# Kernel optimization log

Measured on AMD Instinct MI355X. Metric: run time of the kernel, lower is better.

## Reference

```python
import jax, jax.numpy as jnp
import numpy as np

N = 100000   # nodes
E = 1600000  # edges (avg degree 16)
D = 128      # hidden_dim


def setup_inputs() -> dict:
    key = jax.random.key(0)
    k1, k2, k3, k4, k5, k6 = jax.random.split(key, 6)
    return {
        "t": jnp.zeros((), dtype=jnp.float32),  # unused by the ODE func
        "x": jax.random.normal(k1, (N, D), dtype=jnp.float32),
        "x0": jax.random.normal(k2, (N, D), dtype=jnp.float32),
        "alpha_train": jax.random.normal(k3, (N,), dtype=jnp.float32),
        "adj_values": jax.random.uniform(k4, (E,), dtype=jnp.float32),
        "adj_row": jax.random.randint(k5, (E,), 0, N, dtype=jnp.int32),
        "adj_col": jax.random.randint(k6, (E,), 0, N, dtype=jnp.int32),
    }


def reference(t, x, x0, alpha_train, adj_values, adj_row, adj_col):
    # alph = sigmoid(alpha_train).unsqueeze(1)  -> [N, 1]
    alph = jax.nn.sigmoid(alpha_train)[:, None]
    # ax = spmm(adj, x): COO gather of source-node features, scale by edge
    # value, scatter-add into destination rows. [N, D]
    ax = jax.ops.segment_sum(adj_values[:, None] * x[adj_col], adj_row,
                             num_segments=x.shape[0])
    # f = alph * 0.5 * (ax - x) + x0
    return alph * 0.5 * (ax - x) + x0
```

## Files before the change

### kernel.cpp

```cpp
#include <hip/hip_runtime.h>


#define DIM 128
#define RPB 64
#define RSHIFT 6
#define ACHUNK 4096
#define BCAP 2048
#define NBMAX 2048
#define HISTB 128

typedef float f2v __attribute__((ext_vector_type(2)));

__device__ __forceinline__ float sigmoidf_(float a) {
    return 1.0f / (1.0f + __expf(-a));
}
__device__ __forceinline__ unsigned f2bf(float f) {
    unsigned u = __float_as_uint(f);
    return (u + 0x7FFFu + ((u >> 16) & 1u)) >> 16;
}

__global__ __launch_bounds__(256)
void xcast_hist_kernel(const float* __restrict__ x,
                       unsigned short* __restrict__ xb, int n4,
                       const int* __restrict__ row, int* __restrict__ bhist,
                       int n_edges, int nb, int xg) {
    __shared__ int h[NBMAX];
    if ((int)blockIdx.x < xg) {
        int i = blockIdx.x * 256 + threadIdx.x;
        if (i >= n4) return;
        float4 v = reinterpret_cast<const float4*>(x)[i];
        uint2 o;
        o.x = f2bf(v.x) | (f2bf(v.y) << 16);
        o.y = f2bf(v.z) | (f2bf(v.w) << 16);
        reinterpret_cast<uint2*>(xb)[i] = o;
        return;
    }
    int t = threadIdx.x;
    int bid = blockIdx.x - xg;
    for (int i = t; i < NBMAX; i += 256) h[i] = 0;
    __syncthreads();
    int e4 = n_edges >> 2;
    for (int i = bid * 256 + t; i < e4; i += HISTB * 256) {
        int4 r = reinterpret_cast<const int4*>(row)[i];
        atomicAdd(&h[r.x >> RSHIFT], 1);
        atomicAdd(&h[r.y >> RSHIFT], 1);
        atomicAdd(&h[r.z >> RSHIFT], 1);
        atomicAdd(&h[r.w >> RSHIFT], 1);
    }
    if (bid == 0 && t == 0) {
        for (int i = e4 << 2; i < n_edges; ++i)
            atomicAdd(&bhist[row[i] >> RSHIFT], 1);
    }
    __syncthreads();
    for (int i = t; i < NBMAX; i += 256)
        if (h[i]) atomicAdd(&bhist[i], h[i]);
}

__global__ __launch_bounds__(1024)
void bucket_scan_kernel(const int* __restrict__ bhist, int* __restrict__ boffs,
                        int* __restrict__ bcur, int nb) {
    __shared__ int ts[1024];
    int t = threadIdx.x;
    int i0 = 2 * t, i1 = 2 * t + 1;
    int v0 = (i0 < nb) ? bhist[i0] : 0;
    int v1 = (i1 < nb) ? bhist[i1] : 0;
    ts[t] = v0 + v1;
    __syncthreads();
    for (int off = 1; off < 1024; off <<= 1) {
        int u = (t >= off) ? ts[t - off] : 0;
        __syncthreads();
        ts[t] += u;
        __syncthreads();
    }
    int ex = (t == 0) ? 0 : ts[t - 1];
    if (i0 < nb) { boffs[i0] = ex;      bcur[i0] = ex; }
    if (i1 < nb) { boffs[i1] = ex + v0; bcur[i1] = ex + v0; }
    if (t == 1023) boffs[nb] = ts[1023];
}

__global__ __launch_bounds__(256)
void bin_kernel(const int* __restrict__ row, const int* __restrict__ col,
                const float* __restrict__ vals, int* __restrict__ bcursor,
                int2* __restrict__ epackA, int n_edges, int nb) {
    __shared__ int hist[NBMAX];
    __shared__ int lbase[NBMAX];
    __shared__ int gbase[NBMAX];
    __shared__ int lcur[NBMAX];
    __shared__ int ts[256];
    __shared__ int2 stage[ACHUNK];
    __shared__ unsigned short bkid[ACHUNK];
    int t = threadIdx.x;
    int base = blockIdx.x * ACHUNK;
    int m = n_edges - base;
    if (m > ACHUNK) m = ACHUNK;
    for (int i = t; i < NBMAX; i += 256) hist[i] = 0;
    __syncthreads();
    for (int i = t; i < m; i += 256)
        atomicAdd(&hist[row[base + i] >> RSHIFT], 1);
    __syncthreads();
    int tb = t * 8;
    int hh[8];
    int run = 0;
#pragma unroll
    for (int j = 0; j < 8; ++j) { hh[j] = hist[tb + j]; run += hh[j]; }
    ts[t] = run;
    __syncthreads();
    for (int off = 1; off < 256; off <<= 1) {
        int u = (t >= off) ? ts[t - off] : 0;
        __syncthreads();
        ts[t] += u;
        __syncthreads();
    }
    int ex = (t == 0) ? 0 : ts[t - 1];
#pragma unroll
    for (int j = 0; j < 8; ++j) { lbase[tb + j] = ex; ex += hh[j]; }
    __syncthreads();
    for (int i = t; i < nb; i += 256) {
        int hv = hist[i];
        gbase[i] = hv ? atomicAdd(&bcursor[i], hv) : 0;
        lcur[i] = 0;
    }
    __syncthreads();
    for (int i = t; i < m; i += 256) {
        int r = row[base + i];
        int c = col[base + i];
        float v = vals[base + i];
        int bk = r >> RSHIFT;
        int lp = atomicAdd(&lcur[bk], 1);
        int sp = lbase[bk] + lp;
        stage[sp] = make_int2(((r & (RPB - 1)) << 17) | c, __float_as_int(v));
        bkid[sp] = (unsigned short)bk;
    }
    __syncthreads();
    for (int i = t; i < m; i += 256) {
        int bk = bkid[i];
        epackA[gbase[bk] + (i - lbase[bk])] = stage[i];
    }
}

template <int USE_BF16>
__global__ __launch_bounds__(512)
void fused_sort_gather_kernel(const unsigned short* __restrict__ xb,
                              const float* __restrict__ x,
                              const float* __restrict__ x0,
                              const float* __restrict__ alpha,
                              const int* __restrict__ boffs,
                              const int2* __restrict__ epackA,
                              float* __restrict__ out, int n_nodes) {
    __shared__ int2 eout[BCAP];
    __shared__ int rowstart[RPB];
    __shared__ int rowcur[RPB];
    __shared__ float sval[RPB];
    int b = blockIdx.x, t = threadIdx.x;
    int r0 = b * RPB;
    int begin = boffs[b], end = boffs[b + 1];
    int n = end - begin;
    if (t < RPB) {
        int r = r0 + t;
        sval[t] = (r < n_nodes) ? 0.5f * sigmoidf_(alpha[r]) : 0.f;
        rowstart[t] = 0;
    }
    __syncthreads();
    int wave = t >> 6, lane = t & 63;
    const unsigned* xbp = reinterpret_cast<const unsigned*>(xb);
    const float2* xp = reinterpret_cast<const float2*>(x);
    const f2v* x0v = reinterpret_cast<const f2v*>(x0);
    f2v* outv = reinterpret_cast<f2v*>(out);
    if (n <= BCAP) {
        for (int i = t; i < n; i += 512)
            atomicAdd(&rowstart[epackA[begin + i].x >> 17], 1);
        __syncthreads();
        if (t < RPB) rowcur[t] = rowstart[t];
        __syncthreads();
        for (int off = 1; off < RPB; off <<= 1) {
            int u = (t < RPB && t >= off) ? rowcur[t - off] : 0;
            __syncthreads();
            if (t < RPB) rowcur[t] += u;
            __syncthreads();
        }
        if (t < RPB) {
            int excl = rowcur[t] - rowstart[t];
            rowstart[t] = excl;
            rowcur[t] = excl;
        }
        __syncthreads();
        for (int i = t; i < n; i += 512) {
            int2 e = epackA[begin + i];
            int pos = atomicAdd(&rowcur[e.x >> 17], 1);
            eout[pos] = make_int2(e.x & 0x1FFFF, e.y);
        }
        __syncthreads();
        for (int q = 0; q < 8; ++q) {
            int lr = wave * 8 + q;
            int r = r0 + lr;
            if (r >= n_nodes) break;
            float s = sval[lr];
            int rb = r * 64;
            f2v a0 = __builtin_nontemporal_load(&x0v[rb + lane]);
            float2 acc = make_float2(a0.x, a0.y);
            if (USE_BF16) {
                unsigned dx = xbp[rb + lane];
                acc.x -= s * __uint_as_float((dx & 0xFFFFu) << 16);
                acc.y -= s * __uint_as_float(dx & 0xFFFF0000u);
            } else {
                float2 xv = xp[rb + lane];
                acc.x -= s * xv.x;
                acc.y -= s * xv.y;
            }
            int k = rowstart[lr];
            int stop = (lr + 1 < RPB) ? rowstart[lr + 1] : n;
            for (; k + 8 <= stop; k += 8) {
                float w[8];
                if (USE_BF16) {
                    unsigned d[8];
#pragma unroll
                    for (int j = 0; j < 8; ++j) {
                        int2 e = eout[k + j];
                        w[j] = s * __int_as_float(e.y);
                        d[j] = xbp[(size_t)e.x * 64 + lane];
                    }
#pragma unroll
                    for (int j = 0; j < 8; ++j) {
                        acc.x += w[j] * __uint_as_float((d[j] & 0xFFFFu) << 16);
                        acc.y += w[j] * __uint_as_float(d[j] & 0xFFFF0000u);
                    }
                } else {
                    float2 v[8];
#pragma unroll
                    for (int j = 0; j < 8; ++j) {
                        int2 e = eout[k + j];
                        w[j] = s * __int_as_float(e.y);
                        v[j] = xp[(size_t)e.x * 64 + lane];
                    }
#pragma unroll
                    for (int j = 0; j < 8; ++j) {
                        acc.x += w[j] * v[j].x;
                        acc.y += w[j] * v[j].y;
                    }
                }
            }
            for (; k < stop; ++k) {
                int2 e = eout[k];
                float w = s * __int_as_float(e.y);
                if (USE_BF16) {
                    unsigned d = xbp[(size_t)e.x * 64 + lane];
                    acc.x += w * __uint_as_float((d & 0xFFFFu) << 16);
                    acc.y += w * __uint_as_float(d & 0xFFFF0000u);
                } else {
                    float2 v = xp[(size_t)e.x * 64 + lane];
                    acc.x += w * v.x;
                    acc.y += w * v.y;
                }
            }
            f2v o; o.x = acc.x; o.y = acc.y;
            __builtin_nontemporal_store(o, &outv[rb + lane]);
        }
    } else {
        for (int q = 0; q < 8; ++q) {
            int lr = wave * 8 + q;
            int r = r0 + lr;
            if (r >= n_nodes) break;
            float s = sval[lr];
            int rb = r * 64;
            float2 acc = reinterpret_cast<const float2*>(x0)[rb + lane];
            if (USE_BF16) {
                unsigned dx = xbp[rb + lane];
                acc.x -= s * __uint_as_float((dx & 0xFFFFu) << 16);
                acc.y -= s * __uint_as_float(dx & 0xFFFF0000u);
            } else {
                float2 xv = xp[rb + lane];
                acc.x -= s * xv.x;
                acc.y -= s * xv.y;
            }
            for (int i = 0; i < n; ++i) {
                int2 e = epackA[begin + i];
                if ((e.x >> 17) == lr) {
                    float w = s * __int_as_float(e.y);
                    if (USE_BF16) {
                        unsigned d = xbp[(size_t)(e.x & 0x1FFFF) * 64 + lane];
                        acc.x += w * __uint_as_float((d & 0xFFFFu) << 16);
                        acc.y += w * __uint_as_float(d & 0xFFFF0000u);
                    } else {
                        float2 v = xp[(size_t)(e.x & 0x1FFFF) * 64 + lane];
                        acc.x += w * v.x;
                        acc.y += w * v.y;
                    }
                }
            }
            reinterpret_cast<float2*>(out)[rb + lane] = acc;
        }
    }
}

extern "C" void kernel_launch(void* const* d_in, const int* in_sizes, int n_in,
                              void* d_out, int out_size, void* d_ws, size_t ws_size,
                              hipStream_t stream) {
    const float* x     = (const float*)d_in[1];
    const float* x0    = (const float*)d_in[2];
    const float* alpha = (const float*)d_in[3];
    const float* vals  = (const float*)d_in[4];
    const int*   row   = (const int*)d_in[5];
    const int*   col   = (const int*)d_in[6];
    float* out = (float*)d_out;

    int n_nodes = in_sizes[3];
    int n_edges = in_sizes[4];
    int nb = (n_nodes + RPB - 1) / RPB;

    size_t xb_bytes = (size_t)n_nodes * DIM * sizeof(unsigned short);
    size_t ep_bytes = (size_t)((n_edges + 3) & ~3) * sizeof(int2);
    size_t meta_bytes = (size_t)(NBMAX + NBMAX + 16 + NBMAX) * sizeof(int);
    int use_bf16 = (ws_size >= xb_bytes + ep_bytes + meta_bytes + 512) ? 1 : 0;

    unsigned short* xxb;
    int2* epackA;
    int* bhist;
    if (use_bf16) {
        xxb    = (unsigned short*)d_ws;
        epackA = (int2*)((char*)d_ws + xb_bytes);
        bhist  = (int*)((char*)epackA + ep_bytes);
    } else {
        xxb    = nullptr;
        epackA = (int2*)d_ws;
        bhist  = (int*)((char*)epackA + ep_bytes);
    }
    int* boffs = bhist + NBMAX;
    int* bcur  = boffs + NBMAX + 16;

    hipMemsetAsync(bhist, 0, NBMAX * sizeof(int), stream);

    {
        int n4 = use_bf16 ? ((n_nodes * DIM) >> 2) : 0;
        int xg = use_bf16 ? ((n4 + 255) / 256) : 0;
        xcast_hist_kernel<<<xg + HISTB, 256, 0, stream>>>(
            x, xxb, n4, row, bhist, n_edges, nb, xg);
    }
    bucket_scan_kernel<<<1, 1024, 0, stream>>>(bhist, boffs, bcur, nb);
    {
        int grid = (n_edges + ACHUNK - 1) / ACHUNK;
        bin_kernel<<<grid, 256, 0, stream>>>(row, col, vals, bcur, epackA,
                                             n_edges, nb);
    }
    if (use_bf16) {
        fused_sort_gather_kernel<1><<<nb, 512, 0, stream>>>(
            xxb, x, x0, alpha, boffs, epackA, out, n_nodes);
    } else {
        fused_sort_gather_kernel<0><<<nb, 512, 0, stream>>>(
            xxb, x, x0, alpha, boffs, epackA, out, n_nodes);
    }
}
```

Baseline: 139.8 us.

## Double rows per bucket and stage bucket edges in LDS before sorting

Doubles the rows per bucket to 128, with bucket capacity 4096 and at most 1024 buckets. The gather kernel moves to 1024 threads, each wave still handling 8 rows. Bucket edges are first copied into shared memory with nontemporal loads, so the histogram and the scatter passes read them from LDS instead of reading global memory twice. The scans and bin kernel are adjusted for the smaller bucket count, and the bf16/fp32 branches are hoisted out of the inner loop. The trade-offs are fewer, larger blocks, roughly 64 KB of LDS per block, and more edges per bucket, which may reduce occupancy.

```diff
diff --git a/kernel.cpp b/kernel.cpp
--- a/kernel.cpp
+++ b/kernel.cpp
@@ -2,14 +2,15 @@
 
 
 #define DIM 128
-#define RPB 64
-#define RSHIFT 6
+#define RPB 128
+#define RSHIFT 7
 #define ACHUNK 4096
-#define BCAP 2048
-#define NBMAX 2048
+#define BCAP 4096
+#define NBMAX 1024
 #define HISTB 128
 
 typedef float f2v __attribute__((ext_vector_type(2)));
+typedef int   i2v __attribute__((ext_vector_type(2)));
 
 __device__ __forceinline__ float sigmoidf_(float a) {
     return 1.0f / (1.0f + __expf(-a));
@@ -61,10 +62,7 @@
                         int* __restrict__ bcur, int nb) {
     __shared__ int ts[1024];
     int t = threadIdx.x;
-    int i0 = 2 * t, i1 = 2 * t + 1;
-    int v0 = (i0 < nb) ? bhist[i0] : 0;
-    int v1 = (i1 < nb) ? bhist[i1] : 0;
-    ts[t] = v0 + v1;
+    ts[t] = (t < nb) ? bhist[t] : 0;
     __syncthreads();
     for (int off = 1; off < 1024; off <<= 1) {
         int u = (t >= off) ? ts[t - off] : 0;
@@ -72,9 +70,11 @@
         ts[t] += u;
         __syncthreads();
     }
-    int ex = (t == 0) ? 0 : ts[t - 1];
-    if (i0 < nb) { boffs[i0] = ex;      bcur[i0] = ex; }
-    if (i1 < nb) { boffs[i1] = ex + v0; bcur[i1] = ex + v0; }
+    if (t < nb) {
+        int e = (t == 0) ? 0 : ts[t - 1];
+        boffs[t] = e;
+        bcur[t] = e;
+    }
     if (t == 1023) boffs[nb] = ts[1023];
 }
 
@@ -98,11 +98,11 @@
     for (int i = t; i < m; i += 256)
         atomicAdd(&hist[row[base + i] >> RSHIFT], 1);
     __syncthreads();
-    int tb = t * 8;
-    int hh[8];
+    int tb = t * 4;
+    int hh[4];
     int run = 0;
 #pragma unroll
-    for (int j = 0; j < 8; ++j) { hh[j] = hist[tb + j]; run += hh[j]; }
+    for (int j = 0; j < 4; ++j) { hh[j] = hist[tb + j]; run += hh[j]; }
     ts[t] = run;
     __syncthreads();
     for (int off = 1; off < 256; off <<= 1) {
@@ -113,7 +113,7 @@
     }
     int ex = (t == 0) ? 0 : ts[t - 1];
 #pragma unroll
-    for (int j = 0; j < 8; ++j) { lbase[tb + j] = ex; ex += hh[j]; }
+    for (int j = 0; j < 4; ++j) { lbase[tb + j] = ex; ex += hh[j]; }
     __syncthreads();
     for (int i = t; i < nb; i += 256) {
         int hv = hist[i];
@@ -139,7 +139,7 @@
 }
 
 template <int USE_BF16>
-__global__ __launch_bounds__(512)
+__global__ __launch_bounds__(1024)
 void fused_sort_gather_kernel(const unsigned short* __restrict__ xb,
                               const float* __restrict__ x,
                               const float* __restrict__ x0,
@@ -147,6 +147,7 @@
                               const int* __restrict__ boffs,
                               const int2* __restrict__ epackA,
                               float* __restrict__ out, int n_nodes) {
+    __shared__ int2 ein[BCAP];
     __shared__ int2 eout[BCAP];
     __shared__ int rowstart[RPB];
     __shared__ int rowcur[RPB];
@@ -165,10 +166,16 @@
     const unsigned* xbp = reinterpret_cast<const unsigned*>(xb);
     const float2* xp = reinterpret_cast<const float2*>(x);
     const f2v* x0v = reinterpret_cast<const f2v*>(x0);
+    const i2v* epv = reinterpret_cast<const i2v*>(epackA);
     f2v* outv = reinterpret_cast<f2v*>(out);
     if (n <= BCAP) {
-        for (int i = t; i < n; i += 512)
-            atomicAdd(&rowstart[epackA[begin + i].x >> 17], 1);
+        for (int i = t; i < n; i += 1024) {
+            i2v e = __builtin_nontemporal_load(&epv[begin + i]);
+            ein[i] = make_int2(e.x, e.y);
+        }
+        __syncthreads();
+        for (int i = t; i < n; i += 1024)
+            atomicAdd(&rowstart[ein[i].x >> 17], 1);
         __syncthreads();
         if (t < RPB) rowcur[t] = rowstart[t];
         __syncthreads();
@@ -184,8 +191,8 @@
             rowcur[t] = excl;
         }
         __syncthreads();
-        for (int i = t; i < n; i += 512) {
-            int2 e = epackA[begin + i];
+        for (int i = t; i < n; i += 1024) {
+            int2 e = ein[i];
             int pos = atomicAdd(&rowcur[e.x >> 17], 1);
             eout[pos] = make_int2(e.x & 0x1FFFF, e.y);
         }
@@ -209,10 +216,9 @@
             }
             int k = rowstart[lr];
             int stop = (lr + 1 < RPB) ? rowstart[lr + 1] : n;
-            for (; k + 8 <= stop; k += 8) {
-                float w[8];
-                if (USE_BF16) {
-                    unsigned d[8];
+            if (USE_BF16) {
+                for (; k + 8 <= stop; k += 8) {
+                    unsigned d[8]; float w[8];
 #pragma unroll
                     for (int j = 0; j < 8; ++j) {
                         int2 e = eout[k + j];
@@ -224,8 +230,17 @@
                         acc.x += w[j] * __uint_as_float((d[j] & 0xFFFFu) << 16);
                         acc.y += w[j] * __uint_as_float(d[j] & 0xFFFF0000u);
                     }
-                } else {
-                    float2 v[8];
+                }
+                for (; k < stop; ++k) {
+                    int2 e = eout[k];
+                    float w = s * __int_as_float(e.y);
+                    unsigned d = xbp[(size_t)e.x * 64 + lane];
+                    acc.x += w * __uint_as_float((d & 0xFFFFu) << 16);
+                    acc.y += w * __uint_as_float(d & 0xFFFF0000u);
+                }
+            } else {
+                for (; k + 8 <= stop; k += 8) {
+                    float2 v[8]; float w[8];
 #pragma unroll
                     for (int j = 0; j < 8; ++j) {
                         int2 e = eout[k + j];
@@ -238,15 +253,9 @@
                         acc.y += w[j] * v[j].y;
                     }
                 }
-            }
-            for (; k < stop; ++k) {
-                int2 e = eout[k];
-                float w = s * __int_as_float(e.y);
-                if (USE_BF16) {
-                    unsigned d = xbp[(size_t)e.x * 64 + lane];
-                    acc.x += w * __uint_as_float((d & 0xFFFFu) << 16);
-                    acc.y += w * __uint_as_float(d & 0xFFFF0000u);
-                } else {
+                for (; k < stop; ++k) {
+                    int2 e = eout[k];
+                    float w = s * __int_as_float(e.y);
                     float2 v = xp[(size_t)e.x * 64 + lane];
                     acc.x += w * v.x;
                     acc.y += w * v.y;
@@ -342,10 +351,10 @@
                                              n_edges, nb);
     }
     if (use_bf16) {
-        fused_sort_gather_kernel<1><<<nb, 512, 0, stream>>>(
+        fused_sort_gather_kernel<1><<<nb, 1024, 0, stream>>>(
             xxb, x, x0, alpha, boffs, epackA, out, n_nodes);
     } else {
-        fused_sort_gather_kernel<0><<<nb, 512, 0, stream>>>(
+        fused_sort_gather_kernel<0><<<nb, 1024, 0, stream>>>(
             xxb, x, x0, alpha, boffs, epackA, out, n_nodes);
     }
 }
```

Result: no change. 142.4 us (+1.8%).
